# Kernel optimization log

Hardware: AMD Instinct MI355X
Metric: run time of the kernel (lower is better)

The kernel has to match this reference:

```python
import jax, jax.numpy as jnp
import numpy as np

SEQ, BS, IN, HS = 512, 64, 1024, 1024


def _xavier(key, shape):
    fan_in, fan_out = shape
    limit = np.sqrt(6.0 / (fan_in + fan_out)).astype(np.float32)
    return jax.random.uniform(key, shape, jnp.float32, -limit, limit)


def setup_inputs() -> dict:
    key = jax.random.key(0)
    k1, k2, k3, k4, k5 = jax.random.split(key, 5)
    return {
        "x": jax.random.normal(k1, (SEQ, BS, IN), jnp.float32),
        "h0": jax.random.normal(k2, (1, BS, HS), jnp.float32),
        "c0": jax.random.normal(k3, (1, BS, HS), jnp.float32),
        "weight_ih": _xavier(k4, (IN, 4 * HS)),
        "weight_hh": _xavier(k5, (HS, 4 * HS)),
        "bias": jnp.zeros((4 * HS,), jnp.float32),
    }


def reference(x, h0, c0, weight_ih, weight_hh, bias):
    HSd = weight_hh.shape[0]
    # Precompute the input projection for all timesteps in one big GEMM.
    x_gates = jnp.einsum('sbi,ih->sbh', x, weight_ih) + bias  # [S, B, 4H]

    def step(carry, xg_t):
        h_t, c_t = carry
        gates = xg_t + h_t @ weight_hh  # [B, 4H]
        i_t = jax.nn.sigmoid(gates[:, :HSd])
        f_t = jax.nn.sigmoid(gates[:, HSd:2 * HSd])
        g_t = jnp.tanh(gates[:, 2 * HSd:3 * HSd])
        o_t = jax.nn.sigmoid(gates[:, 3 * HSd:])
        c_t = f_t * c_t + i_t * g_t
        h_t = o_t * jnp.tanh(c_t)
        return (h_t, c_t), h_t

    (h_T, c_T), hidden_seq = jax.lax.scan(step, (h0[0], c0[0]), x_gates)
    return hidden_seq, (h_T[None], c_T[None])
```

## Files before the change

### kernel.cpp

```cpp
#include <hip/hip_runtime.h>
#include <stdint.h>


typedef unsigned short u16;
typedef __attribute__((ext_vector_type(8))) short bf16x8;
typedef __attribute__((ext_vector_type(2))) uint64_t u64x2;
typedef __attribute__((ext_vector_type(4))) float f32x4;

static __device__ __forceinline__ u16 f2b(float f) {
  uint32_t b = __float_as_uint(f);
  return (u16)((b + 0x7fffu + ((b >> 16) & 1u)) >> 16);
}
static __device__ __forceinline__ uint64_t pack4(float4 v) {
  return (uint64_t)f2b(v.x) | ((uint64_t)f2b(v.y) << 16) |
         ((uint64_t)f2b(v.z) << 32) | ((uint64_t)f2b(v.w) << 48);
}
static __device__ __forceinline__ float b2f(u16 u) {
  return __uint_as_float(((uint32_t)u) << 16);
}
static __device__ __forceinline__ float sigm(float x) {
  return 1.0f / (1.0f + __expf(-x));
}
static __device__ __forceinline__ float tanh_(float x) {
  float e = __expf(2.0f * x);
  return 1.0f - 2.0f / (e + 1.0f);
}

__global__ __launch_bounds__(256) void transpose_w(const float* __restrict__ Wih,
                                                   const float* __restrict__ Whh,
                                                   u16* __restrict__ Tih,
                                                   u16* __restrict__ Thh) {
  __shared__ float tile[64][65];
  const float* src = blockIdx.z ? Whh : Wih;
  u16* dst = blockIdx.z ? Thh : Tih;
  int k0 = blockIdx.y * 64, n0 = blockIdx.x * 64;
  int tid = threadIdx.x;
#pragma unroll
  for (int i = 0; i < 16; ++i) {
    int idx = i * 256 + tid;
    int kl = idx >> 6, nl = idx & 63;
    tile[kl][nl] = src[(size_t)(k0 + kl) * 4096 + n0 + nl];
  }
  __syncthreads();
#pragma unroll
  for (int i = 0; i < 16; ++i) {
    int idx = i * 256 + tid;
    int nl = idx >> 6, kl = idx & 63;
    dst[(size_t)(n0 + nl) * 1024 + k0 + kl] = f2b(tile[kl][nl]);
  }
}

__global__ __launch_bounds__(256) void convert_h0(const float* __restrict__ h0,
                                                  u16* __restrict__ dst) {
  int i = blockIdx.x * 256 + threadIdx.x;
  float4 v = ((const float4*)h0)[i];
  ((uint64_t*)dst)[i] = pack4(v);
}

__global__ __launch_bounds__(256) void gemm_xg(const float* __restrict__ A,
                                               const u16* __restrict__ Bt,
                                               const float* __restrict__ bias,
                                               u16* __restrict__ C) {
  __shared__ u16 sA[2][128 * 32];
  __shared__ u16 sB[2][128 * 32];
  const int tid = threadIdx.x;
  const int wave = tid >> 6, lane = tid & 63;
  const int bx = blockIdx.x, by = blockIdx.y;
  const int wr = wave >> 1, wc = wave & 1;
  const int lm = lane & 15, ko = (lane >> 4) * 8;

  const int ar = lane >> 1, ac = (lane & 1) * 16;
  const float* gA = A + (size_t)(by * 128 + wave * 32 + ar) * 1024 + ac;
  const u16* gB = Bt + (size_t)(bx * 128 + wave * 32 + (lane >> 2)) * 1024 + (lane & 3) * 8;
  const int bidx = wave * 1024 + (lane >> 2) * 32 + (lane & 3) * 8;

  f32x4 acc[4][4] = {};

  auto stage = [&](int kt, int buf) {
    const u16* gb = gB + kt * 32;
    bf16x8 b0 = *(const bf16x8*)gb;
    bf16x8 b1 = *(const bf16x8*)(gb + 16 * 1024);
    *(bf16x8*)&sB[buf][bidx] = b0;
    *(bf16x8*)&sB[buf][bidx + 512] = b1;
    const float* ga = gA + kt * 32;
    float4 v0 = *(const float4*)(ga + 0);
    float4 v1 = *(const float4*)(ga + 4);
    float4 v2 = *(const float4*)(ga + 8);
    float4 v3 = *(const float4*)(ga + 12);
    uint64_t* la = (uint64_t*)&sA[buf][wave * 1024 + ar * 32 + ac];
    la[0] = pack4(v0);
    la[1] = pack4(v1);
    la[2] = pack4(v2);
    la[3] = pack4(v3);
  };

  stage(0, 0);
  __syncthreads();
  int p = 0;
  for (int kt = 0; kt < 32; ++kt) {
    if (kt < 31) stage(kt + 1, p ^ 1);
    bf16x8 af[4], bfv[4];
#pragma unroll
    for (int i = 0; i < 4; ++i)
      af[i] = *(const bf16x8*)&sA[p][(wr * 64 + i * 16 + lm) * 32 + ko];
#pragma unroll
    for (int j = 0; j < 4; ++j)
      bfv[j] = *(const bf16x8*)&sB[p][(wc * 64 + j * 16 + lm) * 32 + ko];
#pragma unroll
    for (int i = 0; i < 4; ++i)
#pragma unroll
      for (int j = 0; j < 4; ++j)
        acc[i][j] = __builtin_amdgcn_mfma_f32_16x16x32_bf16(af[i], bfv[j], acc[i][j], 0, 0, 0);
    __syncthreads();
    p ^= 1;
  }

  float bj[4];
#pragma unroll
  for (int j = 0; j < 4; ++j)
    bj[j] = bias[bx * 128 + wc * 64 + j * 16 + lm];
#pragma unroll
  for (int i = 0; i < 4; ++i) {
    int row = by * 128 + wr * 64 + i * 16 + (lane >> 4) * 4;
#pragma unroll
    for (int j = 0; j < 4; ++j) {
      int col = bx * 128 + wc * 64 + j * 16 + lm;
#pragma unroll
      for (int r = 0; r < 4; ++r)
        C[(size_t)(row + r) * 4096 + col] = f2b(acc[i][j][r] + bj[j]);
    }
  }
}

__global__ __launch_bounds__(512, 1) void recur_pers(
    const u16* __restrict__ xg,
    const u16* __restrict__ whh_t,
    u16* __restrict__ h_buf,
    float* __restrict__ c_st,
    float* __restrict__ out_h,
    float* __restrict__ out_hT, float* __restrict__ out_cT,
    uint32_t* __restrict__ flags,
    int t0, int W) {
  __shared__ float xchg[8][4][16][16];

  const int tid = threadIdx.x;
  const int wave = tid >> 6, lane = tid & 63;
  const int bid = blockIdx.x;
  const int ub = bid & 63;
  const int bq = bid >> 6;
  const int lm = lane & 15, ko = (lane >> 4) * 8;

  bf16x8 bfr[4][4];
#pragma unroll
  for (int g = 0; g < 4; ++g) {
    const u16* bp = whh_t + (size_t)(g * 1024 + ub * 16 + lm) * 1024 + wave * 128 + ko;
#pragma unroll
    for (int kc = 0; kc < 4; ++kc) bfr[g][kc] = *(const bf16x8*)(bp + kc * 32);
  }

  const int r_b = tid >> 4, u = tid & 15;
  const int b = bq * 16 + r_b;
  const int unit = ub * 16 + u;
  float c_val = (tid < 256) ? c_st[b * 1024 + unit] : 0.f;

  for (int ts = 0; ts < W; ++ts) {
    const int t = t0 + ts;

    u16 xr0 = 0, xr1 = 0, xr2 = 0, xr3 = 0;
    if (tid < 256) {
      const u16* xgp = xg + ((size_t)ts * 64 + b) * 4096 + unit;
      xr0 = xgp[0];
      xr1 = xgp[1024];
      xr2 = xgp[2048];
      xr3 = xgp[3072];
    }

    const u16* ap = h_buf + (size_t)((t - 1) & 1) * 65536 +
                    (size_t)(bq * 16 + lm) * 1024 + wave * 128 + ko;
    bf16x8 a[4];
#pragma unroll
    for (int kc = 0; kc < 4; ++kc) {
      const uint64_t* p = (const uint64_t*)(ap + kc * 32);
      u64x2 v;
      v.x = __hip_atomic_load(p, __ATOMIC_RELAXED, __HIP_MEMORY_SCOPE_AGENT);
      v.y = __hip_atomic_load(p + 1, __ATOMIC_RELAXED, __HIP_MEMORY_SCOPE_AGENT);
      a[kc] = __builtin_bit_cast(bf16x8, v);
    }

    f32x4 acc[4] = {{0.f, 0.f, 0.f, 0.f},
                    {0.f, 0.f, 0.f, 0.f},
                    {0.f, 0.f, 0.f, 0.f},
                    {0.f, 0.f, 0.f, 0.f}};
#pragma unroll
    for (int kc = 0; kc < 4; ++kc)
#pragma unroll
      for (int g = 0; g < 4; ++g)
        acc[g] = __builtin_amdgcn_mfma_f32_16x16x32_bf16(a[kc], bfr[g][kc], acc[g], 0, 0, 0);

    {
      int crow = (lane >> 4) * 4;
#pragma unroll
      for (int g = 0; g < 4; ++g)
#pragma unroll
        for (int r = 0; r < 4; ++r) xchg[wave][g][crow + r][lm] = acc[g][r];
    }
    __syncthreads();

    float h_new = 0.f;
    if (tid < 256) {
      float raw[4];
#pragma unroll
      for (int g = 0; g < 4; ++g) {
        float s = xchg[0][g][r_b][u];
#pragma unroll
        for (int w = 1; w < 8; ++w) s += xchg[w][g][r_b][u];
        raw[g] = s;
      }
      float ig = sigm(raw[0] + b2f(xr0));
      float fg = sigm(raw[1] + b2f(xr1));
      float gg = tanh_(raw[2] + b2f(xr2));
      float og = sigm(raw[3] + b2f(xr3));
      c_val = fg * c_val + ig * gg;
      h_new = og * tanh_(c_val);
      uint32_t mine = f2b(h_new);
      uint32_t other = __shfl_xor(mine, 1);
      if ((u & 1) == 0) {
        uint32_t pair = mine | (other << 16);
        __hip_atomic_store(
            (uint32_t*)(h_buf + (size_t)(t & 1) * 65536 + (size_t)b * 1024 + unit), pair,
            __ATOMIC_RELAXED, __HIP_MEMORY_SCOPE_AGENT);
      }
      if (t == 511) {
        out_hT[b * 1024 + unit] = h_new;
        out_cT[b * 1024 + unit] = c_val;
      }
    }

    if (ts != W - 1) {
      __syncthreads();
      uint32_t* fl = flags + ((size_t)t * 4 + bq) * 64;
      if (wave == 7) {
        if (lane == 0)
          __hip_atomic_store(fl + ub, 1u, __ATOMIC_RELAXED, __HIP_MEMORY_SCOPE_AGENT);
        uint32_t spin = 0;
        for (; spin < (1u << 15); ++spin) {
          uint32_t v = __hip_atomic_load(fl + lane, __ATOMIC_RELAXED,
                                         __HIP_MEMORY_SCOPE_AGENT);
          if (__all(v == 1u)) break;
          __builtin_amdgcn_s_sleep(1);
        }
        if (spin >= (1u << 15) && lane == 0)
          out_h[(size_t)t * 65536 + bid] = 1.0e6f;
      }
      if (tid < 256) out_h[(size_t)t * 65536 + (size_t)b * 1024 + unit] = h_new;
      __syncthreads();
    } else {
      if (tid < 256) out_h[(size_t)t * 65536 + (size_t)b * 1024 + unit] = h_new;
    }
  }

  if (tid < 256) c_st[b * 1024 + unit] = c_val;
}

extern "C" void kernel_launch(void* const* d_in, const int* in_sizes, int n_in,
                              void* d_out, int out_size, void* d_ws, size_t ws_size,
                              hipStream_t stream) {
  const float* x = (const float*)d_in[0];
  const float* h0 = (const float*)d_in[1];
  const float* c0 = (const float*)d_in[2];
  const float* wih = (const float*)d_in[3];
  const float* whh = (const float*)d_in[4];
  const float* bias = (const float*)d_in[5];

  float* out = (float*)d_out;
  float* out_h = out;
  float* out_hT = out + (size_t)512 * 64 * 1024;
  float* out_cT = out_hT + 64 * 1024;

  const size_t fixed = (size_t)2 * 4096 * 1024 * 2
                       + (size_t)2 * 64 * 1024 * 2
                       + (size_t)64 * 1024 * 4
                       + (size_t)512 * 4 * 64 * 4;
  int W = 64;
  while (W > 4 && fixed + (size_t)W * 64 * 4096 * 2 > ws_size) W >>= 2;

  char* ws = (char*)d_ws;
  u16* wih_t = (u16*)ws;   ws += (size_t)4096 * 1024 * 2;
  u16* whh_t = (u16*)ws;   ws += (size_t)4096 * 1024 * 2;
  u16* xg = (u16*)ws;      ws += (size_t)W * 64 * 4096 * 2;
  u16* h_buf = (u16*)ws;   ws += (size_t)2 * 64 * 1024 * 2;
  float* c_st = (float*)ws; ws += (size_t)64 * 1024 * 4;
  uint32_t* flags = (uint32_t*)ws;

  hipMemsetAsync(flags, 0, (size_t)512 * 4 * 64 * 4, stream);
  convert_h0<<<64, 256, 0, stream>>>(h0, h_buf + 65536);
  hipMemcpyAsync(c_st, c0, (size_t)64 * 1024 * 4, hipMemcpyDeviceToDevice, stream);
  transpose_w<<<dim3(64, 16, 2), 256, 0, stream>>>(wih, whh, wih_t, whh_t);

  for (int t0 = 0; t0 < 512; t0 += W) {
    gemm_xg<<<dim3(32, W / 2), 256, 0, stream>>>(x + (size_t)t0 * 64 * 1024, wih_t, bias, xg);
    int t0c = t0, Wc = W;
    void* args[] = {(void*)&xg,    (void*)&whh_t,  (void*)&h_buf,  (void*)&c_st,
                    (void*)&out_h, (void*)&out_hT, (void*)&out_cT, (void*)&flags,
                    (void*)&t0c,   (void*)&Wc};
    hipLaunchCooperativeKernel((const void*)recur_pers, dim3(256), dim3(512), args, 0,
                               stream);
  }
}
```

Measured before the change: 4.222 ms.

## Interleave two batch quarters per block to hide inter-block barrier latency

Halves the grid to 128 blocks, with each block processing two independent batch quarters in alternating phases. Each phase waits on the previous timestep's flags for its own quarter, then computes and publishes its flag. While one quarter waits on its barrier, the other quarter's work can proceed. The change also moves the out_h store before the barrier and halves the spin timeout. In exchange, the compute per block doubles and only half as many CUs are used.

```diff
diff --git a/kernel.cpp b/kernel.cpp
--- a/kernel.cpp
+++ b/kernel.cpp
@@ -147,7 +147,7 @@
   const int wave = tid >> 6, lane = tid & 63;
   const int bid = blockIdx.x;
   const int ub = bid & 63;
-  const int bq = bid >> 6;
+  const int pair = bid >> 6;
   const int lm = lane & 15, ko = (lane >> 4) * 8;
 
   bf16x8 bfr[4][4];
@@ -159,12 +159,28 @@
   }
 
   const int r_b = tid >> 4, u = tid & 15;
-  const int b = bq * 16 + r_b;
   const int unit = ub * 16 + u;
-  float c_val = (tid < 256) ? c_st[b * 1024 + unit] : 0.f;
-
-  for (int ts = 0; ts < W; ++ts) {
-    const int t = t0 + ts;
+  const int bA = (pair * 2) * 16 + r_b;
+  const int bB = (pair * 2 + 1) * 16 + r_b;
+  float cA = (tid < 256) ? c_st[bA * 1024 + unit] : 0.f;
+  float cB = (tid < 256) ? c_st[bB * 1024 + unit] : 0.f;
+
+  auto phase = [&](int bq, float& c_val, int b, int ts, int t) {
+    if (t > 0) {
+      uint32_t* fl = flags + ((size_t)(t - 1) * 4 + bq) * 64;
+      if (wave == 7) {
+        uint32_t spin = 0;
+        for (; spin < (1u << 14); ++spin) {
+          uint32_t v = __hip_atomic_load(fl + lane, __ATOMIC_RELAXED,
+                                         __HIP_MEMORY_SCOPE_AGENT);
+          if (__all(v == 1u)) break;
+          __builtin_amdgcn_s_sleep(1);
+        }
+        if (spin >= (1u << 14) && lane == 0)
+          out_h[(size_t)t * 65536 + bid] = 1.0e6f;
+      }
+      __syncthreads();
+    }
 
     u16 xr0 = 0, xr1 = 0, xr2 = 0, xr3 = 0;
     if (tid < 256) {
@@ -206,7 +222,6 @@
     }
     __syncthreads();
 
-    float h_new = 0.f;
     if (tid < 256) {
       float raw[4];
 #pragma unroll
@@ -221,45 +236,38 @@
       float gg = tanh_(raw[2] + b2f(xr2));
       float og = sigm(raw[3] + b2f(xr3));
       c_val = fg * c_val + ig * gg;
-      h_new = og * tanh_(c_val);
+      float h_new = og * tanh_(c_val);
       uint32_t mine = f2b(h_new);
       uint32_t other = __shfl_xor(mine, 1);
       if ((u & 1) == 0) {
-        uint32_t pair = mine | (other << 16);
+        uint32_t pairv = mine | (other << 16);
         __hip_atomic_store(
-            (uint32_t*)(h_buf + (size_t)(t & 1) * 65536 + (size_t)b * 1024 + unit), pair,
+            (uint32_t*)(h_buf + (size_t)(t & 1) * 65536 + (size_t)b * 1024 + unit), pairv,
             __ATOMIC_RELAXED, __HIP_MEMORY_SCOPE_AGENT);
       }
+      out_h[(size_t)t * 65536 + (size_t)b * 1024 + unit] = h_new;
       if (t == 511) {
         out_hT[b * 1024 + unit] = h_new;
         out_cT[b * 1024 + unit] = c_val;
       }
     }
 
-    if (ts != W - 1) {
-      __syncthreads();
-      uint32_t* fl = flags + ((size_t)t * 4 + bq) * 64;
-      if (wave == 7) {
-        if (lane == 0)
-          __hip_atomic_store(fl + ub, 1u, __ATOMIC_RELAXED, __HIP_MEMORY_SCOPE_AGENT);
-        uint32_t spin = 0;
-        for (; spin < (1u << 15); ++spin) {
-          uint32_t v = __hip_atomic_load(fl + lane, __ATOMIC_RELAXED,
-                                         __HIP_MEMORY_SCOPE_AGENT);
-          if (__all(v == 1u)) break;
-          __builtin_amdgcn_s_sleep(1);
-        }
-        if (spin >= (1u << 15) && lane == 0)
-          out_h[(size_t)t * 65536 + bid] = 1.0e6f;
-      }
-      if (tid < 256) out_h[(size_t)t * 65536 + (size_t)b * 1024 + unit] = h_new;
-      __syncthreads();
-    } else {
-      if (tid < 256) out_h[(size_t)t * 65536 + (size_t)b * 1024 + unit] = h_new;
-    }
-  }
-
-  if (tid < 256) c_st[b * 1024 + unit] = c_val;
+    __syncthreads();
+    if (wave == 7 && lane == 0)
+      __hip_atomic_store(flags + ((size_t)t * 4 + bq) * 64 + ub, 1u, __ATOMIC_RELAXED,
+                         __HIP_MEMORY_SCOPE_AGENT);
+  };
+
+  for (int ts = 0; ts < W; ++ts) {
+    const int t = t0 + ts;
+    phase(pair * 2, cA, bA, ts, t);
+    phase(pair * 2 + 1, cB, bB, ts, t);
+  }
+
+  if (tid < 256) {
+    c_st[bA * 1024 + unit] = cA;
+    c_st[bB * 1024 + unit] = cB;
+  }
 }
 
 extern "C" void kernel_launch(void* const* d_in, const int* in_sizes, int n_in,
@@ -303,7 +311,7 @@
     void* args[] = {(void*)&xg,    (void*)&whh_t,  (void*)&h_buf,  (void*)&c_st,
                     (void*)&out_h, (void*)&out_hT, (void*)&out_cT, (void*)&flags,
                     (void*)&t0c,   (void*)&Wc};
-    hipLaunchCooperativeKernel((const void*)recur_pers, dim3(256), dim3(512), args, 0,
+    hipLaunchCooperativeKernel((const void*)recur_pers, dim3(128), dim3(512), args, 0,
                                stream);
   }
 }
```

Result: faster. 4.063 ms (-3.8%).

## Split recurrence over 512 four-wave blocks and move flag wait before step

Applied to the files above, without the earlier changes.

Repartitions the persistent LSTM recurrence from 256 blocks of 8 waves into 512 blocks of 4 waves. Each block now handles 8 hidden units across all four gates, with each wave covering 256 of the K dimension, so the cross-wave LDS reduction sums 4 partials instead of 8. The barrier is restructured so each block publishes its flag right after writing h and waits on the previous step's flags at the start of the next step, letting the out_h stores overlap the wait. The cost is twice as many blocks polling twice as many flags per step, and it relies on two blocks being co-resident per CU.

```diff
diff --git a/kernel.cpp b/kernel.cpp
--- a/kernel.cpp
+++ b/kernel.cpp
@@ -132,7 +132,7 @@
   }
 }
 
-__global__ __launch_bounds__(512, 1) void recur_pers(
+__global__ __launch_bounds__(256, 2) void recur_pers(
     const u16* __restrict__ xg,
     const u16* __restrict__ whh_t,
     u16* __restrict__ h_buf,
@@ -141,33 +141,53 @@
     float* __restrict__ out_hT, float* __restrict__ out_cT,
     uint32_t* __restrict__ flags,
     int t0, int W) {
-  __shared__ float xchg[8][4][16][16];
+  __shared__ float xchg[4][16][33];
 
   const int tid = threadIdx.x;
   const int wave = tid >> 6, lane = tid & 63;
   const int bid = blockIdx.x;
-  const int ub = bid & 63;
-  const int bq = bid >> 6;
+  const int ub8 = bid & 127;
+  const int bq = bid >> 7;
   const int lm = lane & 15, ko = (lane >> 4) * 8;
 
-  bf16x8 bfr[4][4];
-#pragma unroll
-  for (int g = 0; g < 4; ++g) {
-    const u16* bp = whh_t + (size_t)(g * 1024 + ub * 16 + lm) * 1024 + wave * 128 + ko;
-#pragma unroll
-    for (int kc = 0; kc < 4; ++kc) bfr[g][kc] = *(const bf16x8*)(bp + kc * 32);
-  }
-
-  const int r_b = tid >> 4, u = tid & 15;
+  bf16x8 bfr[8][2];
+#pragma unroll
+  for (int nt = 0; nt < 2; ++nt) {
+    int c = nt * 16 + lm;
+    const u16* bp =
+        whh_t + (size_t)((c >> 3) * 1024 + ub8 * 8 + (c & 7)) * 1024 + wave * 256 + ko;
+#pragma unroll
+    for (int kk = 0; kk < 8; ++kk) bfr[kk][nt] = *(const bf16x8*)(bp + kk * 32);
+  }
+
+  const int r_b = tid >> 3, u = tid & 7;
   const int b = bq * 16 + r_b;
-  const int unit = ub * 16 + u;
-  float c_val = (tid < 256) ? c_st[b * 1024 + unit] : 0.f;
+  const int unit = ub8 * 8 + u;
+  float c_val = (tid < 128) ? c_st[b * 1024 + unit] : 0.f;
 
   for (int ts = 0; ts < W; ++ts) {
     const int t = t0 + ts;
 
+    if (t > 0) {
+      const uint32_t* fl = flags + ((size_t)(t - 1) * 4 + bq) * 128;
+      if (wave == 3) {
+        uint32_t spin = 0;
+        for (; spin < (1u << 15); ++spin) {
+          uint32_t v0 = __hip_atomic_load(fl + lane, __ATOMIC_RELAXED,
+                                          __HIP_MEMORY_SCOPE_AGENT);
+          uint32_t v1 = __hip_atomic_load(fl + 64 + lane, __ATOMIC_RELAXED,
+                                          __HIP_MEMORY_SCOPE_AGENT);
+          if (__all((v0 == 1u) & (v1 == 1u))) break;
+          __builtin_amdgcn_s_sleep(1);
+        }
+        if (spin >= (1u << 15) && lane == 0)
+          out_h[(size_t)t * 65536 + bid] = 1.0e6f;
+      }
+      __syncthreads();
+    }
+
     u16 xr0 = 0, xr1 = 0, xr2 = 0, xr3 = 0;
-    if (tid < 256) {
+    if (tid < 128) {
       const u16* xgp = xg + ((size_t)ts * 64 + b) * 4096 + unit;
       xr0 = xgp[0];
       xr1 = xgp[1024];
@@ -176,90 +196,72 @@
     }
 
     const u16* ap = h_buf + (size_t)((t - 1) & 1) * 65536 +
-                    (size_t)(bq * 16 + lm) * 1024 + wave * 128 + ko;
-    bf16x8 a[4];
-#pragma unroll
-    for (int kc = 0; kc < 4; ++kc) {
-      const uint64_t* p = (const uint64_t*)(ap + kc * 32);
+                    (size_t)(bq * 16 + lm) * 1024 + wave * 256 + ko;
+    bf16x8 a[8];
+#pragma unroll
+    for (int kk = 0; kk < 8; ++kk) {
+      const uint64_t* p = (const uint64_t*)(ap + kk * 32);
       u64x2 v;
       v.x = __hip_atomic_load(p, __ATOMIC_RELAXED, __HIP_MEMORY_SCOPE_AGENT);
       v.y = __hip_atomic_load(p + 1, __ATOMIC_RELAXED, __HIP_MEMORY_SCOPE_AGENT);
-      a[kc] = __builtin_bit_cast(bf16x8, v);
-    }
-
-    f32x4 acc[4] = {{0.f, 0.f, 0.f, 0.f},
-                    {0.f, 0.f, 0.f, 0.f},
-                    {0.f, 0.f, 0.f, 0.f},
-                    {0.f, 0.f, 0.f, 0.f}};
-#pragma unroll
-    for (int kc = 0; kc < 4; ++kc)
-#pragma unroll
-      for (int g = 0; g < 4; ++g)
-        acc[g] = __builtin_amdgcn_mfma_f32_16x16x32_bf16(a[kc], bfr[g][kc], acc[g], 0, 0, 0);
-
+      a[kk] = __builtin_bit_cast(bf16x8, v);
+    }
+
+    f32x4 acc[2] = {{0.f, 0.f, 0.f, 0.f}, {0.f, 0.f, 0.f, 0.f}};
+#pragma unroll
+    for (int kk = 0; kk < 8; ++kk) {
+#pragma unroll
+      for (int nt = 0; nt < 2; ++nt)
+        acc[nt] = __builtin_amdgcn_mfma_f32_16x16x32_bf16(a[kk], bfr[kk][nt], acc[nt], 0, 0, 0);
+    }
     {
       int crow = (lane >> 4) * 4;
 #pragma unroll
-      for (int g = 0; g < 4; ++g)
-#pragma unroll
-        for (int r = 0; r < 4; ++r) xchg[wave][g][crow + r][lm] = acc[g][r];
+      for (int nt = 0; nt < 2; ++nt)
+#pragma unroll
+        for (int r = 0; r < 4; ++r) xchg[wave][crow + r][nt * 16 + lm] = acc[nt][r];
     }
     __syncthreads();
 
-    float h_new = 0.f;
-    if (tid < 256) {
+    float h_new = 0.f, c_new = 0.f;
+    if (tid < 128) {
       float raw[4];
 #pragma unroll
       for (int g = 0; g < 4; ++g) {
-        float s = xchg[0][g][r_b][u];
-#pragma unroll
-        for (int w = 1; w < 8; ++w) s += xchg[w][g][r_b][u];
-        raw[g] = s;
+        int c = g * 8 + u;
+        raw[g] = xchg[0][r_b][c] + xchg[1][r_b][c] + xchg[2][r_b][c] + xchg[3][r_b][c];
       }
       float ig = sigm(raw[0] + b2f(xr0));
       float fg = sigm(raw[1] + b2f(xr1));
       float gg = tanh_(raw[2] + b2f(xr2));
       float og = sigm(raw[3] + b2f(xr3));
       c_val = fg * c_val + ig * gg;
+      c_new = c_val;
       h_new = og * tanh_(c_val);
       uint32_t mine = f2b(h_new);
       uint32_t other = __shfl_xor(mine, 1);
       if ((u & 1) == 0) {
-        uint32_t pair = mine | (other << 16);
+        uint32_t pairv = mine | (other << 16);
         __hip_atomic_store(
-            (uint32_t*)(h_buf + (size_t)(t & 1) * 65536 + (size_t)b * 1024 + unit), pair,
+            (uint32_t*)(h_buf + (size_t)(t & 1) * 65536 + (size_t)b * 1024 + unit), pairv,
             __ATOMIC_RELAXED, __HIP_MEMORY_SCOPE_AGENT);
       }
+    }
+
+    __syncthreads();
+    if (tid == 0)
+      __hip_atomic_store(flags + ((size_t)t * 4 + bq) * 128 + ub8, 1u, __ATOMIC_RELAXED,
+                         __HIP_MEMORY_SCOPE_AGENT);
+    if (tid < 128) {
+      out_h[(size_t)t * 65536 + (size_t)b * 1024 + unit] = h_new;
       if (t == 511) {
         out_hT[b * 1024 + unit] = h_new;
-        out_cT[b * 1024 + unit] = c_val;
+        out_cT[b * 1024 + unit] = c_new;
       }
     }
-
-    if (ts != W - 1) {
-      __syncthreads();
-      uint32_t* fl = flags + ((size_t)t * 4 + bq) * 64;
-      if (wave == 7) {
-        if (lane == 0)
-          __hip_atomic_store(fl + ub, 1u, __ATOMIC_RELAXED, __HIP_MEMORY_SCOPE_AGENT);
-        uint32_t spin = 0;
-        for (; spin < (1u << 15); ++spin) {
-          uint32_t v = __hip_atomic_load(fl + lane, __ATOMIC_RELAXED,
-                                         __HIP_MEMORY_SCOPE_AGENT);
-          if (__all(v == 1u)) break;
-          __builtin_amdgcn_s_sleep(1);
-        }
-        if (spin >= (1u << 15) && lane == 0)
-          out_h[(size_t)t * 65536 + bid] = 1.0e6f;
-      }
-      if (tid < 256) out_h[(size_t)t * 65536 + (size_t)b * 1024 + unit] = h_new;
-      __syncthreads();
-    } else {
-      if (tid < 256) out_h[(size_t)t * 65536 + (size_t)b * 1024 + unit] = h_new;
-    }
-  }
-
-  if (tid < 256) c_st[b * 1024 + unit] = c_val;
+  }
+
+  if (tid < 128) c_st[b * 1024 + unit] = c_val;
 }
 
 extern "C" void kernel_launch(void* const* d_in, const int* in_sizes, int n_in,
@@ -280,7 +282,7 @@
   const size_t fixed = (size_t)2 * 4096 * 1024 * 2
                        + (size_t)2 * 64 * 1024 * 2
                        + (size_t)64 * 1024 * 4
-                       + (size_t)512 * 4 * 64 * 4;
+                       + (size_t)512 * 4 * 128 * 4;
   int W = 64;
   while (W > 4 && fixed + (size_t)W * 64 * 4096 * 2 > ws_size) W >>= 2;
 
@@ -292,7 +294,7 @@
   float* c_st = (float*)ws; ws += (size_t)64 * 1024 * 4;
   uint32_t* flags = (uint32_t*)ws;
 
-  hipMemsetAsync(flags, 0, (size_t)512 * 4 * 64 * 4, stream);
+  hipMemsetAsync(flags, 0, (size_t)512 * 4 * 128 * 4, stream);
   convert_h0<<<64, 256, 0, stream>>>(h0, h_buf + 65536);
   hipMemcpyAsync(c_st, c0, (size_t)64 * 1024 * 4, hipMemcpyDeviceToDevice, stream);
   transpose_w<<<dim3(64, 16, 2), 256, 0, stream>>>(wih, whh, wih_t, whh_t);
@@ -303,7 +305,7 @@
     void* args[] = {(void*)&xg,    (void*)&whh_t,  (void*)&h_buf,  (void*)&c_st,
                     (void*)&out_h, (void*)&out_hT, (void*)&out_cT, (void*)&flags,
                     (void*)&t0c,   (void*)&Wc};
-    hipLaunchCooperativeKernel((const void*)recur_pers, dim3(256), dim3(512), args, 0,
+    hipLaunchCooperativeKernel((const void*)recur_pers, dim3(512), dim3(256), args, 0,
                                stream);
   }
 }
```

Result: slower. 6.741 ms (+59.7%).

## Replace per-step flag barrier with timestep-tagged h words for dataflow sync

Applied to the files above, without the earlier changes.

Each bf16 pair of h is now stored as a 64-bit word carrying the timestep tag in its upper half. Consumers spin directly on the h values they need until all tags reach the current step, replacing the separate flag array and its all-block barrier with point-to-point dataflow waits. This removes one barrier round-trip and two __syncthreads per step, and the exchange buffer is also padded to reduce LDS bank conflicts. In exchange it doubles the h storage and read traffic, and each wave must poll 16 atomic 64-bit loads per step.

```diff
diff --git a/kernel.cpp b/kernel.cpp
--- a/kernel.cpp
+++ b/kernel.cpp
@@ -51,10 +51,11 @@
 }
 
 __global__ __launch_bounds__(256) void convert_h0(const float* __restrict__ h0,
-                                                  u16* __restrict__ dst) {
+                                                  uint64_t* __restrict__ dst) {
   int i = blockIdx.x * 256 + threadIdx.x;
-  float4 v = ((const float4*)h0)[i];
-  ((uint64_t*)dst)[i] = pack4(v);
+  float2 v = ((const float2*)h0)[i];
+  uint32_t pair = (uint32_t)f2b(v.x) | ((uint32_t)f2b(v.y) << 16);
+  dst[i] = (uint64_t)pair;
 }
 
 __global__ __launch_bounds__(256) void gemm_xg(const float* __restrict__ A,
@@ -135,33 +136,34 @@
 __global__ __launch_bounds__(512, 1) void recur_pers(
     const u16* __restrict__ xg,
     const u16* __restrict__ whh_t,
-    u16* __restrict__ h_buf,
+    uint64_t* __restrict__ h_tag,
     float* __restrict__ c_st,
     float* __restrict__ out_h,
     float* __restrict__ out_hT, float* __restrict__ out_cT,
-    uint32_t* __restrict__ flags,
     int t0, int W) {
-  __shared__ float xchg[8][4][16][16];
+  __shared__ float xchg[8][16][68];
 
   const int tid = threadIdx.x;
   const int wave = tid >> 6, lane = tid & 63;
   const int bid = blockIdx.x;
-  const int ub = bid & 63;
+  const int un = bid & 63;
   const int bq = bid >> 6;
-  const int lm = lane & 15, ko = (lane >> 4) * 8;
+  const int lm = lane & 15, hi = lane >> 4;
 
   bf16x8 bfr[4][4];
 #pragma unroll
-  for (int g = 0; g < 4; ++g) {
-    const u16* bp = whh_t + (size_t)(g * 1024 + ub * 16 + lm) * 1024 + wave * 128 + ko;
-#pragma unroll
-    for (int kc = 0; kc < 4; ++kc) bfr[g][kc] = *(const bf16x8*)(bp + kc * 32);
+  for (int nt = 0; nt < 4; ++nt) {
+    const u16* bp = whh_t + (size_t)(nt * 1024 + un * 16 + lm) * 1024 + wave * 128 + hi * 8;
+#pragma unroll
+    for (int kk = 0; kk < 4; ++kk) bfr[kk][nt] = *(const bf16x8*)(bp + kk * 32);
   }
 
   const int r_b = tid >> 4, u = tid & 15;
   const int b = bq * 16 + r_b;
-  const int unit = ub * 16 + u;
+  const int unit = un * 16 + u;
   float c_val = (tid < 256) ? c_st[b * 1024 + unit] : 0.f;
+
+  const int b_row = bq * 16 + lm;
 
   for (int ts = 0; ts < W; ++ts) {
     const int t = t0 + ts;
@@ -175,45 +177,60 @@
       xr3 = xgp[3072];
     }
 
-    const u16* ap = h_buf + (size_t)((t - 1) & 1) * 65536 +
-                    (size_t)(bq * 16 + lm) * 1024 + wave * 128 + ko;
-    bf16x8 a[4];
-#pragma unroll
-    for (int kc = 0; kc < 4; ++kc) {
-      const uint64_t* p = (const uint64_t*)(ap + kc * 32);
+    const uint64_t* hb = h_tag + ((size_t)((t - 1) & 1) * 64 + b_row) * 512 +
+                         wave * 64 + hi * 4;
+    uint64_t wbuf[16];
+    {
+      uint32_t spin = 0;
+      bool ok = false;
+      for (; spin < (1u << 15); ++spin) {
+#pragma unroll
+        for (int kk = 0; kk < 4; ++kk)
+#pragma unroll
+          for (int j = 0; j < 4; ++j)
+            wbuf[kk * 4 + j] = __hip_atomic_load(hb + kk * 16 + j, __ATOMIC_RELAXED,
+                                                 __HIP_MEMORY_SCOPE_AGENT);
+        bool good = true;
+#pragma unroll
+        for (int i = 0; i < 16; ++i)
+          good &= ((uint32_t)(wbuf[i] >> 32) >= (uint32_t)t);
+        if (__all(good)) { ok = true; break; }
+        __builtin_amdgcn_s_sleep(1);
+      }
+      if (!ok && lane == 0)
+        out_h[(size_t)t * 65536 + bid] = 1.0e6f;
+    }
+
+    f32x4 acc[4] = {};
+#pragma unroll
+    for (int kk = 0; kk < 4; ++kk) {
       u64x2 v;
-      v.x = __hip_atomic_load(p, __ATOMIC_RELAXED, __HIP_MEMORY_SCOPE_AGENT);
-      v.y = __hip_atomic_load(p + 1, __ATOMIC_RELAXED, __HIP_MEMORY_SCOPE_AGENT);
-      a[kc] = __builtin_bit_cast(bf16x8, v);
-    }
-
-    f32x4 acc[4] = {{0.f, 0.f, 0.f, 0.f},
-                    {0.f, 0.f, 0.f, 0.f},
-                    {0.f, 0.f, 0.f, 0.f},
-                    {0.f, 0.f, 0.f, 0.f}};
-#pragma unroll
-    for (int kc = 0; kc < 4; ++kc)
-#pragma unroll
-      for (int g = 0; g < 4; ++g)
-        acc[g] = __builtin_amdgcn_mfma_f32_16x16x32_bf16(a[kc], bfr[g][kc], acc[g], 0, 0, 0);
-
+      v.x = (uint64_t)(uint32_t)wbuf[kk * 4 + 0] |
+            ((uint64_t)(uint32_t)wbuf[kk * 4 + 1] << 32);
+      v.y = (uint64_t)(uint32_t)wbuf[kk * 4 + 2] |
+            ((uint64_t)(uint32_t)wbuf[kk * 4 + 3] << 32);
+      bf16x8 a = __builtin_bit_cast(bf16x8, v);
+#pragma unroll
+      for (int nt = 0; nt < 4; ++nt)
+        acc[nt] = __builtin_amdgcn_mfma_f32_16x16x32_bf16(a, bfr[kk][nt], acc[nt], 0, 0, 0);
+    }
     {
-      int crow = (lane >> 4) * 4;
-#pragma unroll
-      for (int g = 0; g < 4; ++g)
-#pragma unroll
-        for (int r = 0; r < 4; ++r) xchg[wave][g][crow + r][lm] = acc[g][r];
+      int crow = hi * 4;
+#pragma unroll
+      for (int nt = 0; nt < 4; ++nt)
+#pragma unroll
+        for (int r = 0; r < 4; ++r) xchg[wave][crow + r][nt * 16 + lm] = acc[nt][r];
     }
     __syncthreads();
 
-    float h_new = 0.f;
     if (tid < 256) {
       float raw[4];
 #pragma unroll
       for (int g = 0; g < 4; ++g) {
-        float s = xchg[0][g][r_b][u];
-#pragma unroll
-        for (int w = 1; w < 8; ++w) s += xchg[w][g][r_b][u];
+        int c = g * 16 + u;
+        float s = xchg[0][r_b][c];
+#pragma unroll
+        for (int w = 1; w < 8; ++w) s += xchg[w][r_b][c];
         raw[g] = s;
       }
       float ig = sigm(raw[0] + b2f(xr0));
@@ -221,42 +238,22 @@
       float gg = tanh_(raw[2] + b2f(xr2));
       float og = sigm(raw[3] + b2f(xr3));
       c_val = fg * c_val + ig * gg;
-      h_new = og * tanh_(c_val);
+      float h_new = og * tanh_(c_val);
       uint32_t mine = f2b(h_new);
       uint32_t other = __shfl_xor(mine, 1);
       if ((u & 1) == 0) {
-        uint32_t pair = mine | (other << 16);
+        uint64_t word = (uint64_t)(mine | (other << 16)) | ((uint64_t)(uint32_t)(t + 1) << 32);
         __hip_atomic_store(
-            (uint32_t*)(h_buf + (size_t)(t & 1) * 65536 + (size_t)b * 1024 + unit), pair,
+            h_tag + ((size_t)(t & 1) * 64 + b) * 512 + (unit >> 1), word,
             __ATOMIC_RELAXED, __HIP_MEMORY_SCOPE_AGENT);
       }
+      out_h[(size_t)t * 65536 + (size_t)b * 1024 + unit] = h_new;
       if (t == 511) {
         out_hT[b * 1024 + unit] = h_new;
         out_cT[b * 1024 + unit] = c_val;
       }
     }
-
-    if (ts != W - 1) {
-      __syncthreads();
-      uint32_t* fl = flags + ((size_t)t * 4 + bq) * 64;
-      if (wave == 7) {
-        if (lane == 0)
-          __hip_atomic_store(fl + ub, 1u, __ATOMIC_RELAXED, __HIP_MEMORY_SCOPE_AGENT);
-        uint32_t spin = 0;
-        for (; spin < (1u << 15); ++spin) {
-          uint32_t v = __hip_atomic_load(fl + lane, __ATOMIC_RELAXED,
-                                         __HIP_MEMORY_SCOPE_AGENT);
-          if (__all(v == 1u)) break;
-          __builtin_amdgcn_s_sleep(1);
-        }
-        if (spin >= (1u << 15) && lane == 0)
-          out_h[(size_t)t * 65536 + bid] = 1.0e6f;
-      }
-      if (tid < 256) out_h[(size_t)t * 65536 + (size_t)b * 1024 + unit] = h_new;
-      __syncthreads();
-    } else {
-      if (tid < 256) out_h[(size_t)t * 65536 + (size_t)b * 1024 + unit] = h_new;
-    }
+    __syncthreads();
   }
 
   if (tid < 256) c_st[b * 1024 + unit] = c_val;
@@ -278,30 +275,28 @@
   float* out_cT = out_hT + 64 * 1024;
 
   const size_t fixed = (size_t)2 * 4096 * 1024 * 2
-                       + (size_t)2 * 64 * 1024 * 2
-                       + (size_t)64 * 1024 * 4
-                       + (size_t)512 * 4 * 64 * 4;
+                       + (size_t)2 * 64 * 512 * 8
+                       + (size_t)64 * 1024 * 4;
   int W = 64;
   while (W > 4 && fixed + (size_t)W * 64 * 4096 * 2 > ws_size) W >>= 2;
 
   char* ws = (char*)d_ws;
-  u16* wih_t = (u16*)ws;   ws += (size_t)4096 * 1024 * 2;
-  u16* whh_t = (u16*)ws;   ws += (size_t)4096 * 1024 * 2;
-  u16* xg = (u16*)ws;      ws += (size_t)W * 64 * 4096 * 2;
-  u16* h_buf = (u16*)ws;   ws += (size_t)2 * 64 * 1024 * 2;
-  float* c_st = (float*)ws; ws += (size_t)64 * 1024 * 4;
-  uint32_t* flags = (uint32_t*)ws;
-
-  hipMemsetAsync(flags, 0, (size_t)512 * 4 * 64 * 4, stream);
-  convert_h0<<<64, 256, 0, stream>>>(h0, h_buf + 65536);
+  u16* wih_t = (u16*)ws;     ws += (size_t)4096 * 1024 * 2;
+  u16* whh_t = (u16*)ws;     ws += (size_t)4096 * 1024 * 2;
+  u16* xg = (u16*)ws;        ws += (size_t)W * 64 * 4096 * 2;
+  uint64_t* h_tag = (uint64_t*)ws; ws += (size_t)2 * 64 * 512 * 8;
+  float* c_st = (float*)ws;
+
+  hipMemsetAsync(h_tag, 0, (size_t)2 * 64 * 512 * 8, stream);
+  convert_h0<<<128, 256, 0, stream>>>(h0, h_tag + (size_t)64 * 512);
   hipMemcpyAsync(c_st, c0, (size_t)64 * 1024 * 4, hipMemcpyDeviceToDevice, stream);
   transpose_w<<<dim3(64, 16, 2), 256, 0, stream>>>(wih, whh, wih_t, whh_t);
 
   for (int t0 = 0; t0 < 512; t0 += W) {
     gemm_xg<<<dim3(32, W / 2), 256, 0, stream>>>(x + (size_t)t0 * 64 * 1024, wih_t, bias, xg);
     int t0c = t0, Wc = W;
-    void* args[] = {(void*)&xg,    (void*)&whh_t,  (void*)&h_buf,  (void*)&c_st,
-                    (void*)&out_h, (void*)&out_hT, (void*)&out_cT, (void*)&flags,
+    void* args[] = {(void*)&xg,    (void*)&whh_t,  (void*)&h_tag, (void*)&c_st,
+                    (void*)&out_h, (void*)&out_hT, (void*)&out_cT,
                     (void*)&t0c,   (void*)&Wc};
     hipLaunchCooperativeKernel((const void*)recur_pers, dim3(256), dim3(512), args, 0,
                                stream);
```

Result: faster. 4.014 ms (-4.9%).
